# Kernel tuning notes

Measured on AMD Instinct MI355X. Metric: run time of the kernel, lower is better.

The kernel has to match this reference:

```python
import jax, jax.numpy as jnp
import numpy as np

N_NODES = 50000
N_EDGES = 800000
N_FEAT = 128
DIM = 128
N_GRAPHS = 512


def setup_inputs() -> dict:
    key = jax.random.key(0)
    k1, k2, k3, k4, k5, k6 = jax.random.split(key, 6)
    x = jax.random.normal(k1, (N_NODES, N_FEAT), dtype=jnp.float32)
    edge_index = jax.random.randint(k2, (2, N_EDGES), 0, N_NODES, dtype=jnp.int64)
    batch = jnp.sort(jax.random.randint(k3, (N_NODES,), 0, N_GRAPHS, dtype=jnp.int64))
    # GCNConv linear weights (bias=False); stored as [in, out] so h = x @ W
    W1 = jax.random.normal(k4, (N_FEAT, DIM), dtype=jnp.float32) * (1.0 / np.sqrt(N_FEAT))
    W2 = jax.random.normal(k5, (DIM, DIM), dtype=jnp.float32) * (1.0 / np.sqrt(DIM))
    Wfc = jax.random.normal(k6, (DIM, 1), dtype=jnp.float32) * (1.0 / np.sqrt(DIM))
    return {"x": x, "edge_index": edge_index, "batch": batch,
            "W1": W1, "W2": W2, "Wfc": Wfc}


def _gcn_conv(x, W, src, dst):
    # PyG GCNConv with normalize=False, bias=False:
    # linear transform, then scatter-add messages from src into dst.
    h = x @ W                                   # [N, dim]
    return jax.ops.segment_sum(h[src], dst, num_segments=N_NODES)


def reference(x, edge_index, batch, W1, W2, Wfc):
    src, dst = edge_index[0], edge_index[1]
    h = jax.nn.relu(_gcn_conv(x, W1, src, dst))  # conv1 + ReLU
    h = _gcn_conv(h, W2, src, dst)               # conv2
    # global_mean_pool over graph ids
    sums = jax.ops.segment_sum(h, batch, num_segments=N_GRAPHS)          # [G, dim]
    counts = jax.ops.segment_sum(jnp.ones((N_NODES,), h.dtype), batch,
                                 num_segments=N_GRAPHS)                   # [G]
    pooled = sums / jnp.maximum(counts, 1.0)[:, None]
    return jax.nn.sigmoid(pooled @ Wfc)          # [G, 1]
```

## Files before the change

### kernel.cpp

```cpp
#include <hip/hip_runtime.h>

#define N_NODES 50000
#define N_EDGES 800000
#define NF 128
#define N_GRAPHS 512
#define STRIDE 64

#define NBINS 391
#define NBLK 196
#define EPB 4096
#define SC_N (NBINS * NBLK)
#define SC_BLOCKS 38

typedef _Float16 f16;
typedef f16 h2   __attribute__((ext_vector_type(2)));
typedef f16 f16x8 __attribute__((ext_vector_type(8)));
typedef float f32x4 __attribute__((ext_vector_type(4)));

union HU { ushort u; _Float16 h; };
__device__ __forceinline__ float h2f(ushort u) { HU x; x.u = u; return (float)x.h; }
__device__ __forceinline__ ushort f2h(float f) { HU x; x.h = (_Float16)f; return x.u; }

union UH2 { uint u; h2 h; };
__device__ __forceinline__ void acc4h(h2* ah, uint4 u) {
  UH2 c;
  c.u = u.x; ah[0] += c.h;
  c.u = u.y; ah[1] += c.h;
  c.u = u.z; ah[2] += c.h;
  c.u = u.w; ah[3] += c.h;
}

__global__ __launch_bounds__(128) void w2wfc(const float* __restrict__ W2,
                                             const float* __restrict__ Wfc,
                                             float* __restrict__ v) {
  int f = threadIdx.x;
  float s = 0.f;
  for (int j = 0; j < 128; j += 4) {
    float4 w = ((const float4*)(W2 + f * 128))[j >> 2];
    float4 c = ((const float4*)Wfc)[j >> 2];
    s += w.x * c.x + w.y * c.y + w.z * c.z + w.w * c.w;
  }
  v[f] = s;
}

__global__ __launch_bounds__(256) void w1cvt(const float* __restrict__ W1,
                                             ushort* __restrict__ W1T) {
  int i = blockIdx.x * 256 + threadIdx.x;
  int n = i >> 7, k = i & 127;
  W1T[i] = f2h(W1[k * 128 + n]);
}

__global__ __launch_bounds__(256) void bin_count(const int* __restrict__ dst,
                                                 int* __restrict__ bhist) {
  __shared__ int hist[NBINS];
  for (int i = threadIdx.x; i < NBINS; i += 256) hist[i] = 0;
  __syncthreads();
  int e0 = blockIdx.x * EPB;
  int e1 = e0 + EPB; if (e1 > N_EDGES) e1 = N_EDGES;
  for (int e = e0 + threadIdx.x; e < e1; e += 256)
    atomicAdd(&hist[dst[e] >> 7], 1);
  __syncthreads();
  for (int i = threadIdx.x; i < NBINS; i += 256)
    bhist[i * NBLK + blockIdx.x] = hist[i];
}

__device__ __forceinline__ int block_incl_scan_256(int v, int* warp_sums) {
  const int tid = threadIdx.x;
  const int lane = tid & 63;
  const int w = tid >> 6;
#pragma unroll
  for (int off = 1; off < 64; off <<= 1) {
    int t = __shfl_up(v, off, 64);
    if (lane >= off) v += t;
  }
  if (lane == 63) warp_sums[w] = v;
  __syncthreads();
  int ws = 0;
#pragma unroll
  for (int i = 0; i < 4; ++i) ws += (i < w) ? warp_sums[i] : 0;
  return v + ws;
}

__global__ __launch_bounds__(256) void scan_stage1(const int* __restrict__ in,
                                                   int* __restrict__ R,
                                                   int* __restrict__ blocksum) {
  __shared__ int warp_sums[4];
  int tid = threadIdx.x;
  int i0 = blockIdx.x * 2048 + tid * 8;
  int v[8];
  int s = 0;
#pragma unroll
  for (int k = 0; k < 8; ++k) {
    int idx = i0 + k;
    v[k] = (idx < SC_N) ? in[idx] : 0;
    s += v[k];
  }
  int incl = block_incl_scan_256(s, warp_sums);
  int run = incl - s;
#pragma unroll
  for (int k = 0; k < 8; ++k) {
    run += v[k];
    int idx = i0 + k;
    if (idx < SC_N) R[idx + 1] = run;
  }
  if (tid == 255) blocksum[blockIdx.x] = incl;
}

__global__ __launch_bounds__(256) void scan_stage3(int* __restrict__ R,
                                                   const int* __restrict__ blocksum) {
  int i = blockIdx.x * 256 + threadIdx.x;
  if (i < SC_N) {
    int nb = i >> 11;
    int pre = 0;
    for (int j = 0; j < nb; ++j) pre += blocksum[j];
    R[i + 1] += pre;
  }
  if (i == 0) R[0] = 0;
}

__global__ __launch_bounds__(256) void bin_scatter(const int* __restrict__ src,
                                                   const int* __restrict__ dst,
                                                   const int* __restrict__ R,
                                                   uint* __restrict__ ebuf) {
  __shared__ int cur[NBINS];
  for (int i = threadIdx.x; i < NBINS; i += 256) cur[i] = 0;
  __syncthreads();
  int e0 = blockIdx.x * EPB;
  int e1 = e0 + EPB; if (e1 > N_EDGES) e1 = N_EDGES;
  for (int e = e0 + threadIdx.x; e < e1; e += 256) {
    int d = dst[e];
    int b = d >> 7;
    int loc = atomicAdd(&cur[b], 1);
    ebuf[R[b * NBLK + blockIdx.x] + loc] = ((uint)d << 16) | (uint)src[e];
  }
}

__global__ __launch_bounds__(256) void csr_from_bins(const uint* __restrict__ ebuf,
                                                     const int* __restrict__ R,
                                                     int* __restrict__ deg,
                                                     ushort* __restrict__ col16) {
  __shared__ int dl[128];
  const int bin = blockIdx.x;
  const int n0 = bin << 7;
  if (threadIdx.x < 128) dl[threadIdx.x] = 0;
  __syncthreads();
  int j0 = R[bin * NBLK];
  int j1 = R[(bin + 1) * NBLK];
  for (int j = j0 + threadIdx.x; j < j1; j += 256) {
    uint e = ebuf[j];
    int d = (int)(e >> 16);
    int slot = atomicAdd(&dl[d - n0], 1);
    col16[(size_t)d * STRIDE + slot] = (ushort)(e & 0xFFFFu);
  }
  __syncthreads();
  int cnt = N_NODES - n0; if (cnt > 128) cnt = 128;
  if (threadIdx.x < cnt) deg[n0 + threadIdx.x] = dl[threadIdx.x];
}

__global__ __launch_bounds__(256) void gemm_mfma(const float* __restrict__ x,
                                                 const ushort* __restrict__ W1T,
                                                 ushort* __restrict__ y16, int M) {
  const int tid = threadIdx.x;
  const int w = tid >> 6, l = tid & 63;
  const int row0 = blockIdx.x * 64 + w * 16;
  const int mrow = l & 15, kg = l >> 4;
  const int row = row0 + mrow;

  f32x4 acc[8] = {};
  for (int kc = 0; kc < 4; ++kc) {
    const int cb = kc * 32 + kg * 8;
    f16x8 af = {};
    if (row < M) {
      float4 xlo = *(const float4*)(x + (size_t)row * 128 + cb);
      float4 xhi = *(const float4*)(x + (size_t)row * 128 + cb + 4);
      af[0] = (f16)xlo.x; af[1] = (f16)xlo.y; af[2] = (f16)xlo.z; af[3] = (f16)xlo.w;
      af[4] = (f16)xhi.x; af[5] = (f16)xhi.y; af[6] = (f16)xhi.z; af[7] = (f16)xhi.w;
    }
#pragma unroll
    for (int nt = 0; nt < 8; ++nt) {
      uint4 wb = *(const uint4*)(W1T + ((nt * 16 + mrow) << 7) + cb);
      f16x8 bf = *(const f16x8*)&wb;
      acc[nt] = __builtin_amdgcn_mfma_f32_16x16x32_f16(af, bf, acc[nt], 0, 0, 0);
    }
  }
#pragma unroll
  for (int nt = 0; nt < 8; ++nt) {
#pragma unroll
    for (int r = 0; r < 4; ++r) {
      int rr = row0 + kg * 4 + r;
      if (rr < M) y16[(size_t)rr * 128 + nt * 16 + mrow] = f2h(acc[nt][r]);
    }
  }
}

__global__ __launch_bounds__(256) void gather_qdot(const ushort* __restrict__ y16,
                                                   const int* __restrict__ deg,
                                                   const ushort* __restrict__ col16,
                                                   const float* __restrict__ vq,
                                                   float* __restrict__ q) {
  int n = (blockIdx.x * 256 + threadIdx.x) >> 6;
  if (n >= N_NODES) return;
  const int lane = threadIdx.x & 63;
  const int eg = lane >> 4;
  const int fl = lane & 15;

  int dg = deg[n];
  const ushort* cp = col16 + (size_t)n * STRIDE;
  h2 ah[4] = {};

  int j = eg;
  for (; j + 4 < dg; j += 8) {
    int s0 = cp[j], s1 = cp[j + 4];
    uint4 a = ((const uint4*)y16)[(size_t)s0 * 16 + fl];
    uint4 b = ((const uint4*)y16)[(size_t)s1 * 16 + fl];
    acc4h(ah, a);
    acc4h(ah, b);
  }
  if (j < dg) {
    uint4 a = ((const uint4*)y16)[(size_t)cp[j] * 16 + fl];
    acc4h(ah, a);
  }

#pragma unroll
  for (int k = 0; k < 4; ++k) {
    UH2 c, t;
    c.h = ah[k];
    t.u = (uint)__shfl_xor((int)c.u, 16, 64); ah[k] += t.h;
    c.h = ah[k];
    t.u = (uint)__shfl_xor((int)c.u, 32, 64); ah[k] += t.h;
  }
  float4 v0 = ((const float4*)vq)[fl * 2];
  float4 v1 = ((const float4*)vq)[fl * 2 + 1];
  float p = fmaxf((float)ah[0].x, 0.f) * v0.x + fmaxf((float)ah[0].y, 0.f) * v0.y +
            fmaxf((float)ah[1].x, 0.f) * v0.z + fmaxf((float)ah[1].y, 0.f) * v0.w +
            fmaxf((float)ah[2].x, 0.f) * v1.x + fmaxf((float)ah[2].y, 0.f) * v1.y +
            fmaxf((float)ah[3].x, 0.f) * v1.z + fmaxf((float)ah[3].y, 0.f) * v1.w;
  p += __shfl_xor(p, 1, 64);
  p += __shfl_xor(p, 2, 64);
  p += __shfl_xor(p, 4, 64);
  p += __shfl_xor(p, 8, 64);
  if (lane == 0) q[n] = p;
}

__global__ __launch_bounds__(256) void pool_q(const float* __restrict__ q,
                                              const int* __restrict__ deg,
                                              const ushort* __restrict__ col16,
                                              const int* __restrict__ batch,
                                              float* __restrict__ out) {
  __shared__ float red[4];
  int g = blockIdx.x, tid = threadIdx.x;

  int lo = 0, hi = N_NODES;
  while (lo < hi) { int m = (lo + hi) >> 1; if (batch[m] < g) lo = m + 1; else hi = m; }
  int s0 = lo;
  lo = 0; hi = N_NODES;
  while (lo < hi) { int m = (lo + hi) >> 1; if (batch[m] <= g) lo = m + 1; else hi = m; }
  int s1 = lo;

  float sum = 0.f;
  for (int n = s0 + (tid >> 3); n < s1; n += 32) {
    int dg = deg[n];
    const ushort* cp = col16 + (size_t)n * STRIDE;
    for (int j = tid & 7; j < dg; j += 8) sum += q[cp[j]];
  }
#pragma unroll
  for (int off = 32; off > 0; off >>= 1) sum += __shfl_down(sum, off, 64);
  if ((tid & 63) == 0) red[tid >> 6] = sum;
  __syncthreads();
  if (tid == 0) {
    float z = red[0] + red[1] + red[2] + red[3];
    float cnt = fmaxf((float)(s1 - s0), 1.0f);
    z /= cnt;
    out[g] = 1.0f / (1.0f + expf(-z));
  }
}

extern "C" void kernel_launch(void* const* d_in, const int* in_sizes, int n_in,
                              void* d_out, int out_size, void* d_ws, size_t ws_size,
                              hipStream_t stream) {
  const float* x   = (const float*)d_in[0];
  const int*   ei  = (const int*)d_in[1];
  const int*   src = ei;
  const int*   dst = ei + N_EDGES;
  const int* batch = (const int*)d_in[2];
  const float* W1  = (const float*)d_in[3];
  const float* W2  = (const float*)d_in[4];
  const float* Wfc = (const float*)d_in[5];
  float* out = (float*)d_out;

  ushort* y16  = (ushort*)d_ws;
  ushort* col16 = y16 + (size_t)N_NODES * NF;
  int* deg     = (int*)(col16 + (size_t)N_NODES * STRIDE);
  float* q     = (float*)(deg + N_NODES);
  float* v     = q + N_NODES;
  ushort* W1T  = (ushort*)(v + NF + 32);
  uint* ebuf   = (uint*)(W1T + 16384 + 64);
  int* bhist   = (int*)(ebuf + N_EDGES);
  int* R       = bhist + SC_N;
  int* blocksum = R + SC_N + 1;

  const int gemm_grid = (N_NODES + 63) / 64;
  const int gath_grid = (N_NODES * 64 + 255) / 256;
  const int st3_grid  = (SC_N + 255) / 256;

  bin_count<<<NBLK, 256, 0, stream>>>(dst, bhist);
  scan_stage1<<<SC_BLOCKS, 256, 0, stream>>>(bhist, R, blocksum);
  scan_stage3<<<st3_grid, 256, 0, stream>>>(R, blocksum);
  bin_scatter<<<NBLK, 256, 0, stream>>>(src, dst, R, ebuf);
  csr_from_bins<<<NBINS, 256, 0, stream>>>(ebuf, R, deg, col16);

  w2wfc<<<1, 128, 0, stream>>>(W2, Wfc, v);
  w1cvt<<<64, 256, 0, stream>>>(W1, W1T);
  gemm_mfma<<<gemm_grid, 256, 0, stream>>>(x, W1T, y16, N_NODES);

  gather_qdot<<<gath_grid, 256, 0, stream>>>(y16, deg, col16, v, q);

  pool_q<<<N_GRAPHS, 256, 0, stream>>>(q, deg, col16, batch, out);
}
```

Measured before the change: 103.8 us.

## Replace bin count/scan/scatter with fixed-capacity bins and coalesce GEMM output stores

Result: no change. 104.6 us (+0.8%).

```diff
diff --git a/kernel.cpp b/kernel.cpp
--- a/kernel.cpp
+++ b/kernel.cpp
@@ -9,11 +9,10 @@
 #define NBINS 391
 #define NBLK 196
 #define EPB 4096
-#define SC_N (NBINS * NBLK)
-#define SC_BLOCKS 38
+#define BINCAP 2560
 
 typedef _Float16 f16;
-typedef f16 h2   __attribute__((ext_vector_type(2)));
+typedef f16 h2    __attribute__((ext_vector_type(2)));
 typedef f16 f16x8 __attribute__((ext_vector_type(8)));
 typedef float f32x4 __attribute__((ext_vector_type(4)));
 
@@ -50,9 +49,12 @@
   W1T[i] = f2h(W1[k * 128 + n]);
 }
 
-__global__ __launch_bounds__(256) void bin_count(const int* __restrict__ dst,
-                                                 int* __restrict__ bhist) {
+__global__ __launch_bounds__(256) void bin_scatter2(const int* __restrict__ src,
+                                                    const int* __restrict__ dst,
+                                                    int* __restrict__ gcur,
+                                                    uint* __restrict__ ebuf) {
   __shared__ int hist[NBINS];
+  __shared__ int base[NBINS];
   for (int i = threadIdx.x; i < NBINS; i += 256) hist[i] = 0;
   __syncthreads();
   int e0 = blockIdx.x * EPB;
@@ -60,83 +62,22 @@
   for (int e = e0 + threadIdx.x; e < e1; e += 256)
     atomicAdd(&hist[dst[e] >> 7], 1);
   __syncthreads();
-  for (int i = threadIdx.x; i < NBINS; i += 256)
-    bhist[i * NBLK + blockIdx.x] = hist[i];
-}
-
-__device__ __forceinline__ int block_incl_scan_256(int v, int* warp_sums) {
-  const int tid = threadIdx.x;
-  const int lane = tid & 63;
-  const int w = tid >> 6;
-#pragma unroll
-  for (int off = 1; off < 64; off <<= 1) {
-    int t = __shfl_up(v, off, 64);
-    if (lane >= off) v += t;
-  }
-  if (lane == 63) warp_sums[w] = v;
-  __syncthreads();
-  int ws = 0;
-#pragma unroll
-  for (int i = 0; i < 4; ++i) ws += (i < w) ? warp_sums[i] : 0;
-  return v + ws;
-}
-
-__global__ __launch_bounds__(256) void scan_stage1(const int* __restrict__ in,
-                                                   int* __restrict__ R,
-                                                   int* __restrict__ blocksum) {
-  __shared__ int warp_sums[4];
-  int tid = threadIdx.x;
-  int i0 = blockIdx.x * 2048 + tid * 8;
-  int v[8];
-  int s = 0;
-#pragma unroll
-  for (int k = 0; k < 8; ++k) {
-    int idx = i0 + k;
-    v[k] = (idx < SC_N) ? in[idx] : 0;
-    s += v[k];
-  }
-  int incl = block_incl_scan_256(s, warp_sums);
-  int run = incl - s;
-#pragma unroll
-  for (int k = 0; k < 8; ++k) {
-    run += v[k];
-    int idx = i0 + k;
-    if (idx < SC_N) R[idx + 1] = run;
-  }
-  if (tid == 255) blocksum[blockIdx.x] = incl;
-}
-
-__global__ __launch_bounds__(256) void scan_stage3(int* __restrict__ R,
-                                                   const int* __restrict__ blocksum) {
-  int i = blockIdx.x * 256 + threadIdx.x;
-  if (i < SC_N) {
-    int nb = i >> 11;
-    int pre = 0;
-    for (int j = 0; j < nb; ++j) pre += blocksum[j];
-    R[i + 1] += pre;
-  }
-  if (i == 0) R[0] = 0;
-}
-
-__global__ __launch_bounds__(256) void bin_scatter(const int* __restrict__ src,
-                                                   const int* __restrict__ dst,
-                                                   const int* __restrict__ R,
-                                                   uint* __restrict__ ebuf) {
-  __shared__ int cur[NBINS];
-  for (int i = threadIdx.x; i < NBINS; i += 256) cur[i] = 0;
-  __syncthreads();
-  int e0 = blockIdx.x * EPB;
-  int e1 = e0 + EPB; if (e1 > N_EDGES) e1 = N_EDGES;
+  for (int i = threadIdx.x; i < NBINS; i += 256) {
+    int c = hist[i];
+    base[i] = (c > 0) ? atomicAdd(&gcur[i], c) : 0;
+    hist[i] = 0;
+  }
+  __syncthreads();
   for (int e = e0 + threadIdx.x; e < e1; e += 256) {
     int d = dst[e];
     int b = d >> 7;
-    int loc = atomicAdd(&cur[b], 1);
-    ebuf[R[b * NBLK + blockIdx.x] + loc] = ((uint)d << 16) | (uint)src[e];
+    int loc = atomicAdd(&hist[b], 1);
+    ebuf[(size_t)b * BINCAP + base[b] + loc] = ((uint)d << 16) | (uint)src[e];
   }
 }
 
 __global__ __launch_bounds__(256) void csr_from_bins(const uint* __restrict__ ebuf,
-                                                     const int* __restrict__ R,
+                                                     const int* __restrict__ gcur,
                                                      int* __restrict__ deg,
                                                      ushort* __restrict__ col16) {
   __shared__ int dl[128];
@@ -144,9 +85,9 @@
   const int n0 = bin << 7;
   if (threadIdx.x < 128) dl[threadIdx.x] = 0;
   __syncthreads();
-  int j0 = R[bin * NBLK];
-  int j1 = R[(bin + 1) * NBLK];
-  for (int j = j0 + threadIdx.x; j < j1; j += 256) {
+  int cnt_e = gcur[bin];
+  int j0 = bin * BINCAP;
+  for (int j = j0 + threadIdx.x; j < j0 + cnt_e; j += 256) {
     uint e = ebuf[j];
     int d = (int)(e >> 16);
     int slot = atomicAdd(&dl[d - n0], 1);
@@ -160,6 +101,7 @@
 __global__ __launch_bounds__(256) void gemm_mfma(const float* __restrict__ x,
                                                  const ushort* __restrict__ W1T,
                                                  ushort* __restrict__ y16, int M) {
+  __shared__ ushort ly[4][16][136];
   const int tid = threadIdx.x;
   const int w = tid >> 6, l = tid & 63;
   const int row0 = blockIdx.x * 64 + w * 16;
@@ -184,12 +126,18 @@
     }
   }
 #pragma unroll
-  for (int nt = 0; nt < 8; ++nt) {
-#pragma unroll
-    for (int r = 0; r < 4; ++r) {
-      int rr = row0 + kg * 4 + r;
-      if (rr < M) y16[(size_t)rr * 128 + nt * 16 + mrow] = f2h(acc[nt][r]);
-    }
+  for (int nt = 0; nt < 8; ++nt)
+#pragma unroll
+    for (int r = 0; r < 4; ++r)
+      ly[w][kg * 4 + r][nt * 16 + mrow] = f2h(acc[nt][r]);
+  __syncthreads();
+#pragma unroll
+  for (int t = 0; t < 8; ++t) {
+    int idx = t * 64 + l;
+    int r2 = idx >> 5, c2 = idx & 31;
+    int gr = row0 + r2;
+    if (gr < M)
+      ((uint2*)y16)[(size_t)gr * 32 + c2] = *(const uint2*)&ly[w][r2][c2 * 4];
   }
 }
 
@@ -294,20 +242,15 @@
   float* q     = (float*)(deg + N_NODES);
   float* v     = q + N_NODES;
   ushort* W1T  = (ushort*)(v + NF + 32);
-  uint* ebuf   = (uint*)(W1T + 16384 + 64);
-  int* bhist   = (int*)(ebuf + N_EDGES);
-  int* R       = bhist + SC_N;
-  int* blocksum = R + SC_N + 1;
+  int* gcur    = (int*)(W1T + 16384 + 64);
+  uint* ebuf   = (uint*)(gcur + NBINS + 32);
 
   const int gemm_grid = (N_NODES + 63) / 64;
   const int gath_grid = (N_NODES * 64 + 255) / 256;
-  const int st3_grid  = (SC_N + 255) / 256;
-
-  bin_count<<<NBLK, 256, 0, stream>>>(dst, bhist);
-  scan_stage1<<<SC_BLOCKS, 256, 0, stream>>>(bhist, R, blocksum);
-  scan_stage3<<<st3_grid, 256, 0, stream>>>(R, blocksum);
-  bin_scatter<<<NBLK, 256, 0, stream>>>(src, dst, R, ebuf);
-  csr_from_bins<<<NBINS, 256, 0, stream>>>(ebuf, R, deg, col16);
+
+  hipMemsetAsync(gcur, 0, NBINS * sizeof(int), stream);
+  bin_scatter2<<<NBLK, 256, 0, stream>>>(src, dst, gcur, ebuf);
+  csr_from_bins<<<NBINS, 256, 0, stream>>>(ebuf, gcur, deg, col16);
 
   w2wfc<<<1, 128, 0, stream>>>(W2, Wfc, v);
   w1cvt<<<64, 256, 0, stream>>>(W1, W1T);
```
